# Optimization experiments

Measured on AMD Instinct MI355X. Metric: run time of the kernel, lower is better.

The kernel has to match this reference:

```python
import math
import jax, jax.numpy as jnp
import numpy as np

D = 768      # hidden_size
H = 16       # num_attention_heads (hardcoded in module)
DH = D // H  # value dim per head
SEQ = 512    # fpos/tpos are taken modulo 512
EPS = 1e-5   # torch LayerNorm default
SCALE = math.sqrt(D / H)  # attention_head_size = dim_key_query_all / num_heads


def _collab_attn(h, fpos, tpos, Wq, Wk, Wcb, Wv, bv, mix, Wd, bd, lng, lnb):
    """CollaborativeAttention.forward on one segment. h: [SEQ, D]."""
    fpos = fpos % SEQ
    tpos = tpos % SEQ
    fs = h[fpos]                                   # [F, D] gathered 'from' nodes
    ts = h[tpos]                                   # [T, D] gathered 'to' nodes
    q = fs @ Wq.T                                  # [F, D] (no bias)
    k = ts @ Wk.T                                  # [T, D] (no bias)
    mq = q[None, :, :] * mix[:, None, :]           # [H, F, D] per-head mixing
    scores = jnp.einsum('hfd,td->hft', mq, k)      # [H, F, T] full-D contraction
    cb = (ts @ Wcb.T).T                            # [H, T] content bias
    scores = (scores + cb[:, None, :]) / SCALE
    probs = jax.nn.softmax(scores, axis=-1)        # dropout = identity at eval
    v = (ts @ Wv.T + bv).reshape(-1, H, DH).transpose(1, 0, 2)  # [H, T, DH]
    ctx = jnp.einsum('hft,htd->hfd', probs, v)     # [H, F, DH]
    ctx = ctx.transpose(1, 0, 2).reshape(-1, D) @ Wd.T + bd      # [F, D]
    x = fs + ctx                                   # residual on gathered nodes
    mu = x.mean(-1, keepdims=True)
    var = ((x - mu) ** 2).mean(-1, keepdims=True)
    return lng * (x - mu) / jnp.sqrt(var + EPS) + lnb


def _encoder(hidden_states, fpos, tpos, qtoc, ctoq):
    outs = []
    for b in range(3):  # fixed small segment count, matches original unrolling
        o1 = _collab_attn(hidden_states[b], fpos[b], tpos[b], *qtoc).mean(0)
        o2 = _collab_attn(hidden_states[b], tpos[b], fpos[b], *ctoq).mean(0)
        outs.append(jnp.concatenate([o1, o2]))
    return jnp.stack(outs)  # [3, 2*D]


def setup_inputs() -> dict:
    key = jax.random.key(0)
    ks = jax.random.split(key, 32)
    inp = {
        'hidden_states': jax.random.normal(ks[0], (3, SEQ, D), jnp.float32),
        'fpos': jax.random.randint(ks[1], (3, 2048), 0, SEQ, jnp.int32),
        'tpos': jax.random.randint(ks[2], (3, 2048), 0, SEQ, jnp.int32),
    }
    i = 3
    for p in ('qtoc', 'ctoq'):
        for n, shape, std in (('Wq', (D, D), 0.02), ('Wk', (D, D), 0.02),
                              ('Wcb', (H, D), 0.02), ('Wv', (D, D), 0.02),
                              ('Wd', (D, D), 0.02), ('mix', (H, D), 0.2)):
            inp[p + '_' + n] = std * jax.random.normal(ks[i], shape, jnp.float32)
            i += 1
        inp[p + '_bv'] = jnp.zeros((D,), jnp.float32)
        inp[p + '_bd'] = jnp.zeros((D,), jnp.float32)
        inp[p + '_lng'] = jnp.ones((D,), jnp.float32)
        inp[p + '_lnb'] = jnp.zeros((D,), jnp.float32)
    return inp


def reference(hidden_states, fpos, tpos,
              qtoc_Wq, qtoc_Wk, qtoc_Wcb, qtoc_Wv, qtoc_Wd, qtoc_mix,
              qtoc_bv, qtoc_bd, qtoc_lng, qtoc_lnb,
              ctoq_Wq, ctoq_Wk, ctoq_Wcb, ctoq_Wv, ctoq_Wd, ctoq_mix,
              ctoq_bv, ctoq_bd, ctoq_lng, ctoq_lnb):
    qtoc = (qtoc_Wq, qtoc_Wk, qtoc_Wcb, qtoc_Wv, qtoc_bv, qtoc_mix,
            qtoc_Wd, qtoc_bd, qtoc_lng, qtoc_lnb)
    ctoq = (ctoq_Wq, ctoq_Wk, ctoq_Wcb, ctoq_Wv, ctoq_bv, ctoq_mix,
            ctoq_Wd, ctoq_bd, ctoq_lng, ctoq_lnb)
    return _encoder(hidden_states, fpos, tpos, qtoc, ctoq)
```

## Files before the change

kernel.cpp:

```cpp
#include <hip/hip_runtime.h>
#include <math.h>

#define DD 768
#define HH 16
#define DHH 48
#define NPOS 512
#define NIDX 2048
#define INV_SCALE 0.14433756729740643f
#define LN_EPS 1e-5f

typedef __bf16 bf16_t;
typedef __bf16 bf16x8 __attribute__((ext_vector_type(8)));
typedef float f32x4 __attribute__((ext_vector_type(4)));

__device__ __forceinline__ void g2lds16(const void* g, void* l) {
  __builtin_amdgcn_global_load_lds((const __attribute__((address_space(1))) void*)g,
                                   (__attribute__((address_space(3))) void*)l, 16, 0, 0);
}
__device__ __forceinline__ int stg_chunk(int lane) { return (lane & 3) ^ ((lane >> 3) & 3); }
__device__ __forceinline__ int rd_off(int row, int lq) {
  return row * 32 + ((lq ^ ((row >> 1) & 3)) << 3);
}

struct CvtDesc { const float* src; bf16_t* dst; int n8; };
struct CvtBatch { CvtDesc d[13]; };

__global__ __launch_bounds__(256) void prep(const int* __restrict__ fpos,
                                            const int* __restrict__ tpos,
                                            int* __restrict__ CNT, CvtBatch cvb) {
  const int bid = blockIdx.x;
  const int tid = threadIdx.x;
  __shared__ int shist[NPOS];
  if (bid < 6) {
    const int b = bid >> 1, which = bid & 1;
    const int* src = (which ? tpos : fpos) + b * NIDX;
    for (int i = tid; i < NPOS; i += 256) shist[i] = 0;
    __syncthreads();
    for (int i = tid; i < NIDX; i += 256) atomicAdd(&shist[src[i] & (NPOS - 1)], 1);
    __syncthreads();
    for (int i = tid; i < NPOS; i += 256) CNT[bid * NPOS + i] = shist[i];
    return;
  }
  const CvtDesc de = cvb.d[(bid - 6) >> 6];
  for (int i = ((bid - 6) & 63) * 256 + tid; i < de.n8; i += 64 * 256) {
    bf16_t t[8];
    if (de.src) {
      const f32x4 a = *(const f32x4*)(de.src + (size_t)i * 8);
      const f32x4 b = *(const f32x4*)(de.src + (size_t)i * 8 + 4);
#pragma unroll
      for (int e = 0; e < 4; ++e) { t[e] = (bf16_t)a[e]; t[4 + e] = (bf16_t)b[e]; }
    } else {
#pragma unroll
      for (int e = 0; e < 8; ++e) t[e] = (bf16_t)0.f;
    }
    *(bf16x8*)(de.dst + (size_t)i * 8) = *(bf16x8*)t;
  }
}

struct MDesc { const bf16_t* A; const bf16_t* B; const float* bias; void* C;
               float* cb; int mode; int ntiles; };
struct MBatch { MDesc d[18]; };

__global__ __launch_bounds__(256, 4) void gemm64(MBatch batch) {
  const MDesc de = batch.d[blockIdx.y];
  const int mt = blockIdx.x & 7, nt = blockIdx.x >> 3;
  if (nt >= de.ntiles) return;
  const int m0 = mt * 64, n0 = nt * 128;

  __shared__ bf16_t SA[2][2048];
  __shared__ bf16_t SB[2][4096];

  const int tid = threadIdx.x;
  const int w = tid >> 6, lane = tid & 63;
  const int wm = w >> 1, wn = w & 1;
  const int lm = lane & 15, lq = lane >> 4;
  const int sr = lane >> 2, sc = stg_chunk(lane);

  f32x4 acc[2][4] = {};

  auto stage = [&](int buf, int k0) {
#pragma unroll
    for (int c = 0; c < 3; ++c) {
      const int issue = w + c * 4;
      if (issue < 4)
        g2lds16(de.A + (size_t)(m0 + issue * 16 + sr) * 768 + k0 + sc * 8,
                SA[buf] + issue * 512);
      else {
        const int e = issue - 4;
        g2lds16(de.B + (size_t)(n0 + e * 16 + sr) * 768 + k0 + sc * 8,
                SB[buf] + e * 512);
      }
    }
  };

  stage(0, 0);
  for (int k0i = 0; k0i < 24; ++k0i) {
    const int cur = k0i & 1;
    __syncthreads();
    if (k0i + 1 < 24) stage(cur ^ 1, (k0i + 1) * 32);
    bf16x8 af[2], bfr[4];
#pragma unroll
    for (int i = 0; i < 2; ++i)
      af[i] = *(const bf16x8*)(SA[cur] + rd_off(wm * 32 + i * 16 + lm, lq));
#pragma unroll
    for (int j = 0; j < 4; ++j)
      bfr[j] = *(const bf16x8*)(SB[cur] + rd_off(wn * 64 + j * 16 + lm, lq));
#pragma unroll
    for (int i = 0; i < 2; ++i)
#pragma unroll
      for (int j = 0; j < 4; ++j)
        acc[i][j] = __builtin_amdgcn_mfma_f32_16x16x32_bf16(af[i], bfr[j], acc[i][j], 0, 0, 0);
  }

#pragma unroll
  for (int i = 0; i < 2; ++i) {
    const int rbase = m0 + wm * 32 + i * 16 + lq * 4;
#pragma unroll
    for (int j = 0; j < 4; ++j) {
      const int c = n0 + wn * 64 + j * 16 + lm;
      const float bv = (de.bias && c < 768) ? de.bias[c] : 0.f;
#pragma unroll
      for (int r = 0; r < 4; ++r) {
        const float v = acc[i][j][r] + bv;
        if (de.mode == 0)      ((float*)de.C)[(size_t)(rbase + r) * 768 + c] = v;
        else if (de.mode == 1) ((bf16_t*)de.C)[(size_t)(rbase + r) * 768 + c] = (bf16_t)v;
        else if (de.mode == 2) ((bf16_t*)de.C)[(size_t)c * NPOS + rbase + r] = (bf16_t)v;
        else {
          if (c < 768)       ((bf16_t*)de.C)[(size_t)(rbase + r) * 768 + c] = (bf16_t)v;
          else if (c < 784)  de.cb[(size_t)(rbase + r) * 16 + (c - 768)] = v;
        }
      }
    }
  }
}

__global__ __launch_bounds__(256, 4) void attn_mfma(
    const bf16_t* __restrict__ Qg, const bf16_t* __restrict__ Kg,
    const bf16_t* __restrict__ Vt, const float* __restrict__ cbG,
    const int* __restrict__ CNT, const float* __restrict__ mix0,
    const float* __restrict__ mix1, bf16_t* __restrict__ CTX) {
  const int bid = blockIdx.x;
  const int ft = bid & 7, h = (bid >> 3) & 15, pd = bid >> 7;
  const int dir = pd & 1;
  const int f0 = ft * 64;

  __shared__ bf16_t U[17408];
  __shared__ bf16_t mixs[768];
  __shared__ float cbw[512];
  __shared__ float rowl[64];

  const int tid = threadIdx.x;
  const int w = tid >> 6, lane = tid & 63;
  const bf16_t* Qp = Qg + (size_t)pd * NPOS * DD;
  const bf16_t* Kp = Kg + (size_t)pd * NPOS * DD;
  const bf16_t* Vp = Vt + (size_t)pd * DD * NPOS + (size_t)h * DHH * NPOS;
  const float* mix = (dir ? mix1 : mix0) + h * DD;
  const int* cnt = CNT + ((pd & ~1) + (1 - dir)) * NPOS;

  for (int i = tid; i < 768; i += 256) mixs[i] = (bf16_t)(mix[i] * INV_SCALE);
  for (int i = tid; i < 512; i += 256)
    cbw[i] = cbG[((size_t)pd * NPOS + i) * HH + h] * INV_SCALE + __logf((float)cnt[i]);

  const int wm = w >> 1, wn = w & 1;
  const int lm = lane & 15, lq = lane >> 4;
  const int sr = lane >> 2, sc = stg_chunk(lane);

  f32x4 pv[4] = {};

  for (int jt = 0; jt < 4; ++jt) {
    const int j0 = jt * 128;
    __syncthreads();

    auto stage = [&](int buf, int k0) {
#pragma unroll
      for (int c = 0; c < 3; ++c) {
        const int issue = w + c * 4;
        if (issue < 4)
          g2lds16(Qp + (size_t)(f0 + issue * 16 + sr) * DD + k0 + sc * 8,
                  U + buf * 6144 + issue * 512);
        else {
          const int e = issue - 4;
          g2lds16(Kp + (size_t)(j0 + e * 16 + sr) * DD + k0 + sc * 8,
                  U + buf * 6144 + 2048 + e * 512);
        }
      }
    };

    stage(0, 0);
    f32x4 sa[2][4] = {};
    for (int k0i = 0; k0i < 24; ++k0i) {
      const int cur = k0i & 1;
      __syncthreads();
      if (k0i + 1 < 24) stage(cur ^ 1, (k0i + 1) * 32);
      const bf16x8 mx = *(const bf16x8*)&mixs[k0i * 32 + lq * 8];
      bf16x8 af[2], bfr[4];
#pragma unroll
      for (int i = 0; i < 2; ++i) {
        const bf16x8 q = *(const bf16x8*)(U + cur * 6144 + rd_off(wm * 32 + i * 16 + lm, lq));
        bf16_t t[8];
#pragma unroll
        for (int e = 0; e < 8; ++e) t[e] = (bf16_t)(q[e] * mx[e]);
        af[i] = *(bf16x8*)t;
      }
#pragma unroll
      for (int j = 0; j < 4; ++j)
        bfr[j] = *(const bf16x8*)(U + cur * 6144 + 2048 + rd_off(wn * 64 + j * 16 + lm, lq));
#pragma unroll
      for (int i = 0; i < 2; ++i)
#pragma unroll
        for (int j = 0; j < 4; ++j)
          sa[i][j] = __builtin_amdgcn_mfma_f32_16x16x32_bf16(af[i], bfr[j], sa[i][j], 0, 0, 0);
    }
    __syncthreads();

#pragma unroll
    for (int j = 0; j < 4; ++j) {
      const int col = wn * 64 + j * 16 + lm;
      const float cb = cbw[j0 + col];
#pragma unroll
      for (int i = 0; i < 2; ++i) {
        const int rbase = wm * 32 + i * 16 + lq * 4;
#pragma unroll
        for (int r = 0; r < 4; ++r)
          U[(rbase + r) * 136 + col] = (bf16_t)__expf(sa[i][j][r] + cb);
      }
    }
    for (int i = tid; i < 49 * 16; i += 256) {
      const int r = i >> 4, cc = i & 15;
      if (r < 48)
        *(bf16x8*)(U + 8704 + r * 136 + cc * 8) =
            *(const bf16x8*)(Vp + (size_t)r * NPOS + j0 + cc * 8);
      else {
        bf16_t ones[8];
#pragma unroll
        for (int e = 0; e < 8; ++e) ones[e] = (bf16_t)1.f;
        *(bf16x8*)(U + 8704 + 48 * 136 + cc * 8) = *(bf16x8*)ones;
      }
    }
    __syncthreads();

#pragma unroll
    for (int kk = 0; kk < 4; ++kk) {
      const bf16x8 pa = *(const bf16x8*)(U + (w * 16 + lm) * 136 + kk * 32 + lq * 8);
#pragma unroll
      for (int j = 0; j < 4; ++j) {
        const bf16x8 pb = *(const bf16x8*)(U + 8704 + (j * 16 + lm) * 136 + kk * 32 + lq * 8);
        pv[j] = __builtin_amdgcn_mfma_f32_16x16x32_bf16(pa, pb, pv[j], 0, 0, 0);
      }
    }
  }

  if (lm == 0) {
#pragma unroll
    for (int r = 0; r < 4; ++r) rowl[w * 16 + lq * 4 + r] = pv[3][r];
  }
  __syncthreads();
#pragma unroll
  for (int j = 0; j < 3; ++j) {
#pragma unroll
    for (int r = 0; r < 4; ++r) {
      const int fr = w * 16 + lq * 4 + r;
      CTX[((size_t)pd * NPOS + f0 + fr) * DD + h * DHH + j * 16 + lm] =
          (bf16_t)(pv[j][r] / rowl[fr]);
    }
  }
}

__global__ __launch_bounds__(256) void ln_mean_kernel(
    const float* __restrict__ hs, const float* __restrict__ XB,
    const int* __restrict__ CNT,
    const float* __restrict__ lng0, const float* __restrict__ lnb0,
    const float* __restrict__ lng1, const float* __restrict__ lnb1,
    float* __restrict__ out) {
  const int blk = blockIdx.x;
  const int chunk = blk & 63;
  const int pd = blk >> 6;
  const int b = pd >> 1, dir = pd & 1;
  const float* lng = dir ? lng1 : lng0;
  const float* lnb = dir ? lnb1 : lnb0;
  const int* cnt = CNT + pd * NPOS;
  const float* hb = hs + (size_t)b * NPOS * DD;
  const float* xb = XB + (size_t)pd * NPOS * DD;

  __shared__ float wacc[4][DD];
  const int tid = threadIdx.x;
  const int wave = tid >> 6, lane = tid & 63;
  for (int d0 = tid; d0 < 4 * DD; d0 += 256) ((float*)wacc)[d0] = 0.f;
  __syncthreads();

  float lg[12], lb[12];
#pragma unroll
  for (int qd = 0; qd < 12; ++qd) {
    lg[qd] = lng[lane + qd * 64];
    lb[qd] = lnb[lane + qd * 64];
  }

  for (int rr = 0; rr < 2; ++rr) {
    const int p = chunk * 8 + wave * 2 + rr;
    float x[12];
    float s = 0.f, ss = 0.f;
#pragma unroll
    for (int qd = 0; qd < 12; ++qd) {
      const int d0 = lane + qd * 64;
      const float xv = hb[(size_t)p * DD + d0] + xb[(size_t)p * DD + d0];
      x[qd] = xv; s += xv; ss += xv * xv;
    }
#pragma unroll
    for (int o = 1; o < 64; o <<= 1) {
      s += __shfl_xor(s, o);
      ss += __shfl_xor(ss, o);
    }
    const float mu = s * (1.f / 768.f);
    const float var = ss * (1.f / 768.f) - mu * mu;
    const float rstd = rsqrtf(var + LN_EPS);
    const float wgt = (float)cnt[p];
    if (wgt != 0.f) {
#pragma unroll
      for (int qd = 0; qd < 12; ++qd) {
        const int d0 = lane + qd * 64;
        wacc[wave][d0] += wgt * (lg[qd] * (x[qd] - mu) * rstd + lb[qd]);
      }
    }
  }
  __syncthreads();
  for (int d0 = tid; d0 < DD; d0 += 256) {
    const float t = wacc[0][d0] + wacc[1][d0] + wacc[2][d0] + wacc[3][d0];
    atomicAdd(&out[b * 1536 + dir * 768 + d0], t * (1.f / 2048.f));
  }
}

extern "C" void kernel_launch(void* const* d_in, const int* in_sizes, int n_in,
                              void* d_out, int out_size, void* d_ws, size_t ws_size,
                              hipStream_t stream) {
  const float* hs  = (const float*)d_in[0];
  const int* fpos  = (const int*)d_in[1];
  const int* tpos  = (const int*)d_in[2];

  const float* Wq[2]; const float* Wk[2]; const float* Wcb[2]; const float* Wv[2];
  const float* Wd[2]; const float* mixp[2];
  const float* bv[2]; const float* bd[2]; const float* lng[2]; const float* lnb[2];
  for (int p = 0; p < 2; ++p) {
    const int base = 3 + p * 10;
    Wq[p]   = (const float*)d_in[base + 0];
    Wk[p]   = (const float*)d_in[base + 1];
    Wcb[p]  = (const float*)d_in[base + 2];
    Wv[p]   = (const float*)d_in[base + 3];
    Wd[p]   = (const float*)d_in[base + 4];
    mixp[p] = (const float*)d_in[base + 5];
    bv[p]   = (const float*)d_in[base + 6];
    bd[p]   = (const float*)d_in[base + 7];
    lng[p]  = (const float*)d_in[base + 8];
    lnb[p]  = (const float*)d_in[base + 9];
  }

  char* wsp = (char*)d_ws;
  size_t off = 0;
  auto alloc = [&](size_t bytes) { char* p = wsp + off; off = (off + bytes + 255) & ~(size_t)255; return p; };
  bf16_t* hsb  = (bf16_t*)alloc((size_t)3 * NPOS * DD * 2);
  bf16_t* Wb   = (bf16_t*)alloc((size_t)6 * DD * DD * 2);
  bf16_t* WkCb = (bf16_t*)alloc((size_t)2 * 896 * DD * 2);
  bf16_t* Qbf  = (bf16_t*)alloc((size_t)6 * NPOS * DD * 2);
  bf16_t* Kbf  = (bf16_t*)alloc((size_t)6 * NPOS * DD * 2);
  bf16_t* VtG  = (bf16_t*)alloc((size_t)6 * DD * NPOS * 2);
  bf16_t* CTXb = (bf16_t*)alloc((size_t)6 * NPOS * DD * 2);
  float*  XB   = (float*) alloc((size_t)6 * NPOS * DD * 4);
  float*  cbG  = (float*) alloc((size_t)6 * NPOS * HH * 4);
  int*    CNTb = (int*)   alloc((size_t)6 * NPOS * 4);

  hipMemsetAsync(d_out, 0, (size_t)out_size * sizeof(float), stream);

  CvtBatch cvb{};
  cvb.d[0] = CvtDesc{hs, hsb, 3 * NPOS * DD / 8};
  for (int p = 0; p < 2; ++p) {
    cvb.d[1 + p * 3] = CvtDesc{Wq[p], Wb + (size_t)(p * 3 + 0) * DD * DD, DD * DD / 8};
    cvb.d[2 + p * 3] = CvtDesc{Wv[p], Wb + (size_t)(p * 3 + 1) * DD * DD, DD * DD / 8};
    cvb.d[3 + p * 3] = CvtDesc{Wd[p], Wb + (size_t)(p * 3 + 2) * DD * DD, DD * DD / 8};
    bf16_t* wk = WkCb + (size_t)p * 896 * DD;
    cvb.d[7 + p * 3] = CvtDesc{Wk[p], wk, DD * DD / 8};
    cvb.d[8 + p * 3] = CvtDesc{Wcb[p], wk + (size_t)768 * DD, 16 * DD / 8};
    cvb.d[9 + p * 3] = CvtDesc{nullptr, wk + (size_t)784 * DD, 112 * DD / 8};
  }
  prep<<<838, 256, 0, stream>>>(fpos, tpos, CNTb, cvb);

  MBatch gb{};
  int n = 0;
  for (int b = 0; b < 3; ++b)
    for (int p = 0; p < 2; ++p) {
      const int pd = b * 2 + p;
      const bf16_t* A = hsb + (size_t)b * NPOS * DD;
      const size_t o = (size_t)pd * NPOS * DD;
      gb.d[n++] = MDesc{A, Wb + (size_t)(p * 3 + 0) * DD * DD, nullptr, Qbf + o, nullptr, 1, 6};
      gb.d[n++] = MDesc{A, WkCb + (size_t)p * 896 * DD, nullptr, Kbf + o,
                        cbG + (size_t)pd * NPOS * HH, 3, 7};
      gb.d[n++] = MDesc{A, Wb + (size_t)(p * 3 + 1) * DD * DD, bv[p],
                        VtG + (size_t)pd * DD * NPOS, nullptr, 2, 6};
    }
  gemm64<<<dim3(56, 18), 256, 0, stream>>>(gb);

  attn_mfma<<<768, 256, 0, stream>>>(Qbf, Kbf, VtG, cbG, CNTb, mixp[0], mixp[1], CTXb);

  MBatch gd{};
  for (int b = 0; b < 3; ++b)
    for (int p = 0; p < 2; ++p) {
      const int pd = b * 2 + p;
      const size_t o = (size_t)pd * NPOS * DD;
      gd.d[pd] = MDesc{CTXb + o, Wb + (size_t)(p * 3 + 2) * DD * DD, bd[p],
                       XB + o, nullptr, 0, 6};
    }
  gemm64<<<dim3(56, 6), 256, 0, stream>>>(gd);

  ln_mean_kernel<<<384, 256, 0, stream>>>(hs, XB, CNTb, lng[0], lnb[0], lng[1], lnb[1],
                                          (float*)d_out);
}
```

Baseline: 245.8 us.

## Restructure attention blocks to share K tiles across two heads

The attention kernel now runs 512 threads per block. Each block handles 32 query rows for a pair of heads over all 512 keys, instead of 64 rows for one head in four key tiles. Each staged Q/K slice feeds two head-specific mix scalings, and the full score row is written to LDS once before a two-half P·V pass. V and a ones-row for the softmax normaliser are staged into a separate LDS buffer. The previous double-buffered K/Q staging is dropped in favour of load-sync-compute per k step, so load latency is no longer hidden. LDS use per block also grows.

```diff
diff --git a/kernel.cpp b/kernel.cpp
--- a/kernel.cpp
+++ b/kernel.cpp
@@ -134,134 +134,145 @@
   }
 }
 
-__global__ __launch_bounds__(256, 4) void attn_mfma(
+__global__ __launch_bounds__(512, 4) void attn_mfma(
     const bf16_t* __restrict__ Qg, const bf16_t* __restrict__ Kg,
     const bf16_t* __restrict__ Vt, const float* __restrict__ cbG,
     const int* __restrict__ CNT, const float* __restrict__ mix0,
     const float* __restrict__ mix1, bf16_t* __restrict__ CTX) {
   const int bid = blockIdx.x;
-  const int ft = bid & 7, h = (bid >> 3) & 15, pd = bid >> 7;
+  const int pd = bid >> 7;
+  const int hg = (bid >> 4) & 7;
+  const int ft = bid & 15;
   const int dir = pd & 1;
-  const int f0 = ft * 64;
+  const int f0 = ft * 32;
 
   __shared__ bf16_t U[17408];
-  __shared__ bf16_t mixs[768];
-  __shared__ float cbw[512];
-  __shared__ float rowl[64];
+  __shared__ bf16_t Vs[64 * 264];
+  __shared__ float mixs[2][768];
+  __shared__ float cbw[2][512];
+  __shared__ float rowl[2][32];
 
   const int tid = threadIdx.x;
   const int w = tid >> 6, lane = tid & 63;
+  const int hh = w & 1, jq = w >> 1;
+  const int lm = lane & 15, lq = lane >> 4;
+  const int sr = lane >> 2, sc = stg_chunk(lane);
+
   const bf16_t* Qp = Qg + (size_t)pd * NPOS * DD;
   const bf16_t* Kp = Kg + (size_t)pd * NPOS * DD;
-  const bf16_t* Vp = Vt + (size_t)pd * DD * NPOS + (size_t)h * DHH * NPOS;
-  const float* mix = (dir ? mix1 : mix0) + h * DD;
+  const float* mixsel = dir ? mix1 : mix0;
   const int* cnt = CNT + ((pd & ~1) + (1 - dir)) * NPOS;
 
-  for (int i = tid; i < 768; i += 256) mixs[i] = (bf16_t)(mix[i] * INV_SCALE);
-  for (int i = tid; i < 512; i += 256)
-    cbw[i] = cbG[((size_t)pd * NPOS + i) * HH + h] * INV_SCALE + __logf((float)cnt[i]);
-
-  const int wm = w >> 1, wn = w & 1;
-  const int lm = lane & 15, lq = lane >> 4;
-  const int sr = lane >> 2, sc = stg_chunk(lane);
-
-  f32x4 pv[4] = {};
-
-  for (int jt = 0; jt < 4; ++jt) {
-    const int j0 = jt * 128;
+  for (int i = tid; i < 2 * 768; i += 512) {
+    const int h2 = i / 768, c = i % 768;
+    mixs[h2][c] = mixsel[(hg * 2 + h2) * DD + c] * INV_SCALE;
+  }
+  for (int i = tid; i < 2 * 512; i += 512) {
+    const int h2 = i >> 9, j = i & 511;
+    cbw[h2][j] = cbG[((size_t)pd * NPOS + j) * HH + hg * 2 + h2] * INV_SCALE
+               + __logf((float)cnt[j]);
+  }
+  for (int i = tid; i < 16 * 264; i += 512) {
+    const int r = 48 + i / 264, c = i % 264;
+    Vs[r * 264 + c] = (bf16_t)((r == 48 && c < 256) ? 1.f : 0.f);
+  }
+
+  f32x4 sa[2][8] = {};
+
+  for (int k0i = 0; k0i < 24; ++k0i) {
+    const int k0 = k0i * 32;
     __syncthreads();
-
-    auto stage = [&](int buf, int k0) {
-#pragma unroll
-      for (int c = 0; c < 3; ++c) {
-        const int issue = w + c * 4;
-        if (issue < 4)
-          g2lds16(Qp + (size_t)(f0 + issue * 16 + sr) * DD + k0 + sc * 8,
-                  U + buf * 6144 + issue * 512);
-        else {
-          const int e = issue - 4;
-          g2lds16(Kp + (size_t)(j0 + e * 16 + sr) * DD + k0 + sc * 8,
-                  U + buf * 6144 + 2048 + e * 512);
+#pragma unroll
+    for (int c = 0; c < 5; ++c) {
+      const int issue = w + c * 8;
+      if (issue < 2)
+        g2lds16(Qp + (size_t)(f0 + issue * 16 + sr) * DD + k0 + sc * 8,
+                U + issue * 512);
+      else if (issue < 34) {
+        const int e = issue - 2;
+        g2lds16(Kp + (size_t)(e * 16 + sr) * DD + k0 + sc * 8,
+                U + 1024 + e * 512);
+      }
+    }
+    __syncthreads();
+
+    const f32x4 mxa = *(const f32x4*)&mixs[hh][k0 + lq * 8];
+    const f32x4 mxb = *(const f32x4*)&mixs[hh][k0 + lq * 8 + 4];
+    bf16x8 af[2];
+#pragma unroll
+    for (int i = 0; i < 2; ++i) {
+      const bf16x8 q = *(const bf16x8*)(U + rd_off(i * 16 + lm, lq));
+      bf16_t t[8];
+#pragma unroll
+      for (int e = 0; e < 4; ++e) {
+        t[e]     = (bf16_t)((float)q[e] * mxa[e]);
+        t[4 + e] = (bf16_t)((float)q[4 + e] * mxb[e]);
+      }
+      af[i] = *(bf16x8*)t;
+    }
+#pragma unroll
+    for (int jj = 0; jj < 8; ++jj) {
+      const bf16x8 bf = *(const bf16x8*)(U + 1024 + rd_off(jq * 128 + jj * 16 + lm, lq));
+      sa[0][jj] = __builtin_amdgcn_mfma_f32_16x16x32_bf16(af[0], bf, sa[0][jj], 0, 0, 0);
+      sa[1][jj] = __builtin_amdgcn_mfma_f32_16x16x32_bf16(af[1], bf, sa[1][jj], 0, 0, 0);
+    }
+  }
+  __syncthreads();
+
+  const int fi = w & 1, cj = w >> 1;
+  f32x4 pv[2] = {};
+
+  for (int ph = 0; ph < 2; ++ph) {
+    const int h = hg * 2 + ph;
+    const bf16_t* Vp = Vt + (size_t)pd * DD * NPOS + (size_t)h * DHH * NPOS;
+
+    if (hh == ph) {
+#pragma unroll
+      for (int jj = 0; jj < 8; ++jj) {
+        const int col = jq * 128 + jj * 16 + lm;
+        const float cb = cbw[ph][col];
+#pragma unroll
+        for (int i = 0; i < 2; ++i) {
+          const int rb = i * 16 + lq * 4;
+#pragma unroll
+          for (int r = 0; r < 4; ++r)
+            U[(rb + r) * 532 + col] = (bf16_t)__expf(sa[i][jj][r] + cb);
         }
       }
-    };
-
-    stage(0, 0);
-    f32x4 sa[2][4] = {};
-    for (int k0i = 0; k0i < 24; ++k0i) {
-      const int cur = k0i & 1;
+    }
+
+    for (int vh = 0; vh < 2; ++vh) {
+      for (int i = tid; i < 48 * 32; i += 512) {
+        const int r = i >> 5, cc = i & 31;
+        *(bf16x8*)(Vs + r * 264 + cc * 8) =
+            *(const bf16x8*)(Vp + (size_t)r * NPOS + vh * 256 + cc * 8);
+      }
       __syncthreads();
-      if (k0i + 1 < 24) stage(cur ^ 1, (k0i + 1) * 32);
-      const bf16x8 mx = *(const bf16x8*)&mixs[k0i * 32 + lq * 8];
-      bf16x8 af[2], bfr[4];
-#pragma unroll
-      for (int i = 0; i < 2; ++i) {
-        const bf16x8 q = *(const bf16x8*)(U + cur * 6144 + rd_off(wm * 32 + i * 16 + lm, lq));
-        bf16_t t[8];
-#pragma unroll
-        for (int e = 0; e < 8; ++e) t[e] = (bf16_t)(q[e] * mx[e]);
-        af[i] = *(bf16x8*)t;
-      }
-#pragma unroll
-      for (int j = 0; j < 4; ++j)
-        bfr[j] = *(const bf16x8*)(U + cur * 6144 + 2048 + rd_off(wn * 64 + j * 16 + lm, lq));
-#pragma unroll
-      for (int i = 0; i < 2; ++i)
-#pragma unroll
-        for (int j = 0; j < 4; ++j)
-          sa[i][j] = __builtin_amdgcn_mfma_f32_16x16x32_bf16(af[i], bfr[j], sa[i][j], 0, 0, 0);
-    }
-    __syncthreads();
-
-#pragma unroll
-    for (int j = 0; j < 4; ++j) {
-      const int col = wn * 64 + j * 16 + lm;
-      const float cb = cbw[j0 + col];
-#pragma unroll
-      for (int i = 0; i < 2; ++i) {
-        const int rbase = wm * 32 + i * 16 + lq * 4;
-#pragma unroll
-        for (int r = 0; r < 4; ++r)
-          U[(rbase + r) * 136 + col] = (bf16_t)__expf(sa[i][j][r] + cb);
-      }
-    }
-    for (int i = tid; i < 49 * 16; i += 256) {
-      const int r = i >> 4, cc = i & 15;
-      if (r < 48)
-        *(bf16x8*)(U + 8704 + r * 136 + cc * 8) =
-            *(const bf16x8*)(Vp + (size_t)r * NPOS + j0 + cc * 8);
-      else {
-        bf16_t ones[8];
-#pragma unroll
-        for (int e = 0; e < 8; ++e) ones[e] = (bf16_t)1.f;
-        *(bf16x8*)(U + 8704 + 48 * 136 + cc * 8) = *(bf16x8*)ones;
-      }
-    }
-    __syncthreads();
-
-#pragma unroll
-    for (int kk = 0; kk < 4; ++kk) {
-      const bf16x8 pa = *(const bf16x8*)(U + (w * 16 + lm) * 136 + kk * 32 + lq * 8);
-#pragma unroll
-      for (int j = 0; j < 4; ++j) {
-        const bf16x8 pb = *(const bf16x8*)(U + 8704 + (j * 16 + lm) * 136 + kk * 32 + lq * 8);
-        pv[j] = __builtin_amdgcn_mfma_f32_16x16x32_bf16(pa, pb, pv[j], 0, 0, 0);
-      }
-    }
-  }
-
-  if (lm == 0) {
-#pragma unroll
-    for (int r = 0; r < 4; ++r) rowl[w * 16 + lq * 4 + r] = pv[3][r];
+#pragma unroll
+      for (int kk = 0; kk < 8; ++kk) {
+        const bf16x8 pa = *(const bf16x8*)(U + (fi * 16 + lm) * 532 + vh * 256 + kk * 32 + lq * 8);
+        const bf16x8 pb = *(const bf16x8*)(Vs + (cj * 16 + lm) * 264 + kk * 32 + lq * 8);
+        pv[ph] = __builtin_amdgcn_mfma_f32_16x16x32_bf16(pa, pb, pv[ph], 0, 0, 0);
+      }
+      __syncthreads();
+    }
+    if (cj == 3 && lm == 0) {
+#pragma unroll
+      for (int r = 0; r < 4; ++r) rowl[ph][fi * 16 + lq * 4 + r] = pv[ph][r];
+    }
   }
   __syncthreads();
-#pragma unroll
-  for (int j = 0; j < 3; ++j) {
-#pragma unroll
-    for (int r = 0; r < 4; ++r) {
-      const int fr = w * 16 + lq * 4 + r;
-      CTX[((size_t)pd * NPOS + f0 + fr) * DD + h * DHH + j * 16 + lm] =
-          (bf16_t)(pv[j][r] / rowl[fr]);
+
+  if (cj < 3) {
+#pragma unroll
+    for (int ph = 0; ph < 2; ++ph) {
+      const int h = hg * 2 + ph;
+#pragma unroll
+      for (int r = 0; r < 4; ++r) {
+        const int fr = fi * 16 + lq * 4 + r;
+        CTX[((size_t)pd * NPOS + f0 + fr) * DD + h * DHH + cj * 16 + lm] =
+            (bf16_t)(pv[ph][r] / rowl[ph][fr]);
+      }
     }
   }
 }
@@ -397,7 +408,7 @@
     }
   gemm64<<<dim3(56, 18), 256, 0, stream>>>(gb);
 
-  attn_mfma<<<768, 256, 0, stream>>>(Qbf, Kbf, VtG, cbG, CNTb, mixp[0], mixp[1], CTXb);
+  attn_mfma<<<768, 512, 0, stream>>>(Qbf, Kbf, VtG, cbG, CNTb, mixp[0], mixp[1], CTXb);
 
   MBatch gd{};
   for (int b = 0; b < 3; ++b)
```

New measurement: 250.0 us. About the same (+1.7%).
